# Optimization experiments

Measured on AMD Instinct MI355X. Metric: run time of the kernel, lower is better.

The kernel has to match this reference:

```python
import jax, jax.numpy as jnp
from jax import lax
import numpy as np

B, D, L = 32, 64, 4096
E = 8          # num_experts
K = 2          # top-k
OC = 32        # out_channels


def setup_inputs() -> dict:
    key = jax.random.key(0)
    ks = jax.random.split(key, 6)
    x = jax.random.normal(ks[0], (B, D, L), dtype=jnp.float32)
    # gating weight [D*5, E] (torch init is zeros; use small random for a meaningful reference)
    w_gate = jax.random.normal(ks[1], (D * 5, E), dtype=jnp.float32) * 0.02
    # Conv1d(D -> OC, kernel 3)
    conv1_w = jax.random.normal(ks[2], (OC, D, 3), dtype=jnp.float32) * (1.0 / np.sqrt(D * 3))
    conv1_b = jax.random.normal(ks[3], (OC,), dtype=jnp.float32) * 0.01
    # Conv1d(OC -> OC*E, kernel 1)
    conv2_w = jax.random.normal(ks[4], (OC * E, OC, 1), dtype=jnp.float32) * (1.0 / np.sqrt(OC))
    conv2_b = jax.random.normal(ks[5], (OC * E,), dtype=jnp.float32) * 0.01
    return {"x": x, "w_gate": w_gate, "conv1_w": conv1_w, "conv1_b": conv1_b,
            "conv2_w": conv2_w, "conv2_b": conv2_b}


def _gates(g_in, w_gate):
    # eval-mode noisy_top_k_gating: no noise, softmax -> top-(k+1) -> renormalize top-k -> scatter
    logits = jax.nn.softmax(g_in @ w_gate, axis=1)            # [B, E]
    top_v, top_i = lax.top_k(logits, min(K + 1, E))           # sorted descending
    vk = top_v[:, :K]
    ik = top_i[:, :K]
    gk = vk / (jnp.sum(vk, axis=1, keepdims=True) + 1e-6)
    gates = jnp.zeros_like(logits).at[jnp.arange(logits.shape[0])[:, None], ik].set(gk)
    return gates


def reference(x, w_gate, conv1_w, conv1_b, conv2_w, conv2_b):
    b, d, l = x.shape
    g_in = x[:, :, -6:-1].reshape(b, d * 5)                   # last-5-timestep gating features
    gates = _gates(g_in, w_gate)                              # [B, E]
    dn = ("NCH", "OIH", "NCH")
    h = lax.conv_general_dilated(x, conv1_w, (1,), "VALID", dimension_numbers=dn)
    h = jnp.tanh(h + conv1_b[None, :, None])                  # [B, OC, L-2]
    out = lax.conv_general_dilated(h, conv2_w, (1,), "VALID", dimension_numbers=dn)
    out = out + conv2_b[None, :, None]                        # [B, OC*E, L']
    lp = out.shape[-1]
    out = out.transpose(0, 2, 1).reshape(b, lp, OC, E)        # [B, L', OC, E]
    moe = jnp.einsum("blde,be->bld", out, gates)              # weighted combine
    return moe.transpose(0, 2, 1)                             # [B, OC, L']
```

## Files before the change

kernel.cpp:

```cpp
#include <hip/hip_runtime.h>
#include <math.h>

#define B_  32
#define D_  64
#define L_  4096
#define E_  8
#define OC_ 32
#define LP_ 4094
#define TILE 128
#define NT   32

typedef __attribute__((ext_vector_type(8)))  short short8;
typedef __attribute__((ext_vector_type(16))) float float16;

static __device__ __forceinline__ unsigned cvtpk(float a, float b) {
    unsigned r;
    asm("v_cvt_pk_bf16_f32 %0, %1, %2" : "=v"(r) : "v"(a), "v"(b));
    return r;
}
static __device__ __forceinline__ float fast_tanh(float x) {
    float e = __expf(2.0f * x);
    return fmaf(-2.0f, __builtin_amdgcn_rcpf(e + 1.0f), 1.0f);
}

__global__ __launch_bounds__(256, 4)
void fused_all(const float* __restrict__ x,
               const float* __restrict__ w_gate,
               const float* __restrict__ c1w,
               const float* __restrict__ c1b,
               const float* __restrict__ c2w,
               const float* __restrict__ c2b,
               float* __restrict__ out)
{
    __shared__ __align__(16) unsigned short xT[130 * 64];
    __shared__ __align__(16) unsigned short aFl[12 * 64 * 8];

    const int tid  = threadIdx.x;
    const int lane = tid & 63;
    const int wv   = tid >> 6;
    const int b    = blockIdx.x >> 5;
    const int l0   = (blockIdx.x & 31) << 7;
    const float* xb = x + (size_t)b * (D_ * L_);

    {
        const int c2 = tid >> 3;
        const int jb = (tid & 7) << 2;
        const float* p0 = xb + (size_t)(2 * c2) * L_ + l0;
        const float* p1 = p0 + L_;
        #pragma unroll
        for (int jq = 0; jq < 4; ++jq) {
            int j = jq * 32 + jb;
            float4 v0 = *(const float4*)(p0 + j);
            float4 v1 = *(const float4*)(p1 + j);
            float e0[4] = {v0.x, v0.y, v0.z, v0.w};
            float e1[4] = {v1.x, v1.y, v1.z, v1.w};
            #pragma unroll
            for (int r = 0; r < 4; ++r) {
                int row = j + r;
                int off = (row * 128 + c2 * 4) ^ ((row & 7) << 4);
                *(unsigned*)((char*)xT + off) = cvtpk(e0[r], e1[r]);
            }
        }
        if (tid < 64) {
            int cc2 = tid >> 1, jj = tid & 1;
            int row = TILE + jj;
            int lg  = l0 + row;
            float f0 = 0.f, f1 = 0.f;
            if (lg < L_) {
                f0 = xb[(size_t)(2 * cc2) * L_ + lg];
                f1 = xb[(size_t)(2 * cc2 + 1) * L_ + lg];
            }
            int off = (row * 128 + cc2 * 4) ^ ((row & 7) << 4);
            *(unsigned*)((char*)xT + off) = cvtpk(f0, f1);
        }
    }

    {
        const int oc = tid >> 3;
        const int c0 = (tid & 7) << 3;
        const float* wp = c1w + oc * 192 + c0 * 3;
        float v[24];
        #pragma unroll
        for (int q = 0; q < 6; ++q)
            *(float4*)(v + 4 * q) = *(const float4*)(wp + 4 * q);
        const int ksoff = c0 >> 4;
        const int half  = (c0 >> 3) & 1;
        #pragma unroll
        for (int t = 0; t < 3; ++t) {
            union { short8 s8; unsigned u[4]; } w8;
            #pragma unroll
            for (int jj = 0; jj < 4; ++jj)
                w8.u[jj] = cvtpk(v[(2 * jj) * 3 + t], v[(2 * jj + 1) * 3 + t]);
            int base = ((t * 4 + ksoff) * 64 + half * 32 + oc) * 8;
            *(short8*)(aFl + base) = w8.s8;
        }
    }

    int i0, i1;
    float g0, g1;
    {
        const int d = lane;
        float part[E_];
        #pragma unroll
        for (int e = 0; e < E_; ++e) part[e] = 0.f;
        #pragma unroll
        for (int t = 0; t < 5; ++t) {
            float xvt = xb[(size_t)d * L_ + (L_ - 6) + t];
            const float* wgp = w_gate + (d * 5 + t) * E_;
            float4 wa = *(const float4*)wgp;
            float4 wb = *(const float4*)(wgp + 4);
            part[0] = fmaf(xvt, wa.x, part[0]);
            part[1] = fmaf(xvt, wa.y, part[1]);
            part[2] = fmaf(xvt, wa.z, part[2]);
            part[3] = fmaf(xvt, wa.w, part[3]);
            part[4] = fmaf(xvt, wb.x, part[4]);
            part[5] = fmaf(xvt, wb.y, part[5]);
            part[6] = fmaf(xvt, wb.z, part[6]);
            part[7] = fmaf(xvt, wb.w, part[7]);
        }
        #pragma unroll
        for (int off = 1; off < 64; off <<= 1) {
            #pragma unroll
            for (int e = 0; e < E_; ++e)
                part[e] += __shfl_xor(part[e], off, 64);
        }
        float m = part[0];
        #pragma unroll
        for (int e = 1; e < E_; ++e) m = fmaxf(m, part[e]);
        float p[E_], s = 0.f;
        #pragma unroll
        for (int e = 0; e < E_; ++e) { p[e] = expf(part[e] - m); s += p[e]; }
        float inv = 1.f / s;
        #pragma unroll
        for (int e = 0; e < E_; ++e) p[e] *= inv;

        i0 = 0;
        #pragma unroll
        for (int e = 1; e < E_; ++e) if (p[e] > p[i0]) i0 = e;
        i1 = (i0 == 0) ? 1 : 0;
        #pragma unroll
        for (int e = 0; e < E_; ++e) {
            if (e == i0) continue;
            if (p[e] > p[i1]) i1 = e;
        }
        const float v0 = p[i0], v1 = p[i1];
        const float den = v0 + v1 + 1e-6f;
        g0 = v0 / den;
        g1 = v1 / den;
    }

    const int cl = lane & 31;
    const int hi = lane >> 5;

    short8 a2[2];
    #pragma unroll
    for (int ks = 0; ks < 2; ++ks) {
        const float* q0 = c2w + (cl * E_ + i0) * OC_ + ks * 16 + hi * 8;
        const float* q1 = c2w + (cl * E_ + i1) * OC_ + ks * 16 + hi * 8;
        float4 u0a = *(const float4*)q0, u0b = *(const float4*)(q0 + 4);
        float4 u1a = *(const float4*)q1, u1b = *(const float4*)(q1 + 4);
        union { short8 s8; unsigned u[4]; } f;
        f.u[0] = cvtpk(fmaf(g0, u0a.x, g1 * u1a.x), fmaf(g0, u0a.y, g1 * u1a.y));
        f.u[1] = cvtpk(fmaf(g0, u0a.z, g1 * u1a.z), fmaf(g0, u0a.w, g1 * u1a.w));
        f.u[2] = cvtpk(fmaf(g0, u0b.x, g1 * u1b.x), fmaf(g0, u0b.y, g1 * u1b.y));
        f.u[3] = cvtpk(fmaf(g0, u0b.z, g1 * u1b.z), fmaf(g0, u0b.w, g1 * u1b.w));
        a2[ks] = f.s8;
    }

    __syncthreads();

    const int cb = wv * 32;
    float16 acc = (float16)0.0f;
    #pragma unroll
    for (int t = 0; t < 3; ++t) {
        int row = cb + cl + t;
        int rb  = row * 128;
        int swz = (row & 7) << 4;
        #pragma unroll
        for (int q = 0; q < 4; ++q) {
            short8 af = *(const short8*)(aFl + ((t * 4 + q) * 64 + lane) * 8);
            int off = (rb + q * 32 + hi * 16) ^ swz;
            short8 bf = *(const short8*)((const char*)xT + off);
            acc = __builtin_amdgcn_mfma_f32_32x32x16_bf16(af, bf, acc, 0, 0, 0);
        }
    }

    float th[16];
    #pragma unroll
    for (int r = 0; r < 16; ++r) {
        int row = (r & 3) + 8 * (r >> 2) + 4 * hi;
        th[r] = fast_tanh(acc[r] + c1b[row]);
    }

    unsigned x0a = hi ? cvtpk(th[0],  th[1])  : cvtpk(th[4],  th[5]);
    unsigned x0b = hi ? cvtpk(th[2],  th[3])  : cvtpk(th[6],  th[7]);
    unsigned x1a = hi ? cvtpk(th[8],  th[9])  : cvtpk(th[12], th[13]);
    unsigned x1b = hi ? cvtpk(th[10], th[11]) : cvtpk(th[14], th[15]);
    unsigned r0a = (unsigned)__shfl_xor((int)x0a, 32, 64);
    unsigned r0b = (unsigned)__shfl_xor((int)x0b, 32, 64);
    unsigned r1a = (unsigned)__shfl_xor((int)x1a, 32, 64);
    unsigned r1b = (unsigned)__shfl_xor((int)x1b, 32, 64);

    union U { short8 s8; unsigned u[4]; };
    U b0, b1;
    b0.u[0] = hi ? r0a : cvtpk(th[0], th[1]);
    b0.u[1] = hi ? r0b : cvtpk(th[2], th[3]);
    b0.u[2] = hi ? cvtpk(th[4], th[5]) : r0a;
    b0.u[3] = hi ? cvtpk(th[6], th[7]) : r0b;
    b1.u[0] = hi ? r1a : cvtpk(th[8], th[9]);
    b1.u[1] = hi ? r1b : cvtpk(th[10], th[11]);
    b1.u[2] = hi ? cvtpk(th[12], th[13]) : r1a;
    b1.u[3] = hi ? cvtpk(th[14], th[15]) : r1b;

    float16 acc2 = (float16)0.0f;
    acc2 = __builtin_amdgcn_mfma_f32_32x32x16_bf16(a2[0], b0.s8, acc2, 0, 0, 0);
    acc2 = __builtin_amdgcn_mfma_f32_32x32x16_bf16(a2[1], b1.s8, acc2, 0, 0, 0);

    int l = l0 + cb + cl;
    if (l < LP_) {
        float* ob = out + (size_t)b * (OC_ * (size_t)LP_) + l;
        #pragma unroll
        for (int r = 0; r < 16; ++r) {
            int row = (r & 3) + 8 * (r >> 2) + 4 * hi;
            float bb = fmaf(g0, c2b[row * E_ + i0], g1 * c2b[row * E_ + i1]);
            ob[(size_t)row * LP_] = acc2[r] + bb;
        }
    }
}

extern "C" void kernel_launch(void* const* d_in, const int* in_sizes, int n_in,
                              void* d_out, int out_size, void* d_ws, size_t ws_size,
                              hipStream_t stream)
{
    const float* x      = (const float*)d_in[0];
    const float* w_gate = (const float*)d_in[1];
    const float* c1w    = (const float*)d_in[2];
    const float* c1b    = (const float*)d_in[3];
    const float* c2w    = (const float*)d_in[4];
    const float* c2b    = (const float*)d_in[5];
    float* out = (float*)d_out;

    fused_all<<<B_ * NT, 256, 0, stream>>>(x, w_gate, c1w, c1b, c2w, c2b, out);
}
```

Baseline: 22.75 us.

## Issue all global loads up front and compute gating on one wave via LDS

All global loads of the x tile, the halo and the conv1 weights are issued into registers at kernel start, before the gating computation, so their latency overlaps the gating math. The gating softmax/top-k and the mixing of the conv2 weights now run only on wave 0, with the results shared to the other waves through LDS instead of being computed redundantly by every wave. The conv1 A-fragments are preloaded from LDS into registers before the MFMA loop. This raises register pressure, which could lower occupancy, and adds LDS traffic for broadcasting the gate values.

```diff
diff --git a/kernel.cpp b/kernel.cpp
--- a/kernel.cpp
+++ b/kernel.cpp
@@ -7,8 +7,6 @@
 #define E_  8
 #define OC_ 32
 #define LP_ 4094
-#define TILE 128
-#define NT   32
 
 typedef __attribute__((ext_vector_type(8)))  short short8;
 typedef __attribute__((ext_vector_type(16))) float float16;
@@ -32,8 +30,11 @@
                const float* __restrict__ c2b,
                float* __restrict__ out)
 {
-    __shared__ __align__(16) unsigned short xT[130 * 64];
+    __shared__ __align__(16) unsigned short xT[132 * 64];
     __shared__ __align__(16) unsigned short aFl[12 * 64 * 8];
+    __shared__ __align__(16) unsigned short a2L[2 * 64 * 8];
+    __shared__ float gF[2];
+    __shared__ int   gI[2];
 
     const int tid  = threadIdx.x;
     const int lane = tid & 63;
@@ -42,63 +43,38 @@
     const int l0   = (blockIdx.x & 31) << 7;
     const float* xb = x + (size_t)b * (D_ * L_);
 
+    const int c2 = tid >> 3;
+    const int jb = (tid & 7) << 2;
+    const float* p0 = xb + (size_t)(2 * c2) * L_ + l0;
+    const float* p1 = p0 + L_;
+    float4 A0[4], A1[4];
+    #pragma unroll
+    for (int jq = 0; jq < 4; ++jq) {
+        int j = jq * 32 + jb;
+        A0[jq] = *(const float4*)(p0 + j);
+        A1[jq] = *(const float4*)(p1 + j);
+    }
+    float hA0 = 0.f, hA1 = 0.f;
+    const int haloc = tid >> 1, haloj = tid & 1;
+    if (tid < 64) {
+        int lg = l0 + 128 + haloj;
+        if (lg < L_) {
+            hA0 = xb[(size_t)(2 * haloc) * L_ + lg];
+            hA1 = xb[(size_t)(2 * haloc + 1) * L_ + lg];
+        }
+    }
+
+    const int w_oc = tid >> 3;
+    const int w_c0 = (tid & 7) << 3;
+    float wv24[24];
     {
-        const int c2 = tid >> 3;
-        const int jb = (tid & 7) << 2;
-        const float* p0 = xb + (size_t)(2 * c2) * L_ + l0;
-        const float* p1 = p0 + L_;
-        #pragma unroll
-        for (int jq = 0; jq < 4; ++jq) {
-            int j = jq * 32 + jb;
-            float4 v0 = *(const float4*)(p0 + j);
-            float4 v1 = *(const float4*)(p1 + j);
-            float e0[4] = {v0.x, v0.y, v0.z, v0.w};
-            float e1[4] = {v1.x, v1.y, v1.z, v1.w};
-            #pragma unroll
-            for (int r = 0; r < 4; ++r) {
-                int row = j + r;
-                int off = (row * 128 + c2 * 4) ^ ((row & 7) << 4);
-                *(unsigned*)((char*)xT + off) = cvtpk(e0[r], e1[r]);
-            }
-        }
-        if (tid < 64) {
-            int cc2 = tid >> 1, jj = tid & 1;
-            int row = TILE + jj;
-            int lg  = l0 + row;
-            float f0 = 0.f, f1 = 0.f;
-            if (lg < L_) {
-                f0 = xb[(size_t)(2 * cc2) * L_ + lg];
-                f1 = xb[(size_t)(2 * cc2 + 1) * L_ + lg];
-            }
-            int off = (row * 128 + cc2 * 4) ^ ((row & 7) << 4);
-            *(unsigned*)((char*)xT + off) = cvtpk(f0, f1);
-        }
-    }
-
-    {
-        const int oc = tid >> 3;
-        const int c0 = (tid & 7) << 3;
-        const float* wp = c1w + oc * 192 + c0 * 3;
-        float v[24];
+        const float* wp = c1w + w_oc * 192 + w_c0 * 3;
         #pragma unroll
         for (int q = 0; q < 6; ++q)
-            *(float4*)(v + 4 * q) = *(const float4*)(wp + 4 * q);
-        const int ksoff = c0 >> 4;
-        const int half  = (c0 >> 3) & 1;
-        #pragma unroll
-        for (int t = 0; t < 3; ++t) {
-            union { short8 s8; unsigned u[4]; } w8;
-            #pragma unroll
-            for (int jj = 0; jj < 4; ++jj)
-                w8.u[jj] = cvtpk(v[(2 * jj) * 3 + t], v[(2 * jj + 1) * 3 + t]);
-            int base = ((t * 4 + ksoff) * 64 + half * 32 + oc) * 8;
-            *(short8*)(aFl + base) = w8.s8;
-        }
-    }
-
-    int i0, i1;
-    float g0, g1;
-    {
+            *(float4*)(wv24 + 4 * q) = *(const float4*)(wp + 4 * q);
+    }
+
+    if (wv == 0) {
         const int d = lane;
         float part[E_];
         #pragma unroll
@@ -134,10 +110,10 @@
         #pragma unroll
         for (int e = 0; e < E_; ++e) p[e] *= inv;
 
-        i0 = 0;
+        int i0 = 0;
         #pragma unroll
         for (int e = 1; e < E_; ++e) if (p[e] > p[i0]) i0 = e;
-        i1 = (i0 == 0) ? 1 : 0;
+        int i1 = (i0 == 0) ? 1 : 0;
         #pragma unroll
         for (int e = 0; e < E_; ++e) {
             if (e == i0) continue;
@@ -145,29 +121,73 @@
         }
         const float v0 = p[i0], v1 = p[i1];
         const float den = v0 + v1 + 1e-6f;
-        g0 = v0 / den;
-        g1 = v1 / den;
-    }
+        const float g0 = v0 / den, g1 = v1 / den;
+
+        const int cl0 = lane & 31;
+        const int hi0 = lane >> 5;
+        #pragma unroll
+        for (int ks = 0; ks < 2; ++ks) {
+            const float* q0 = c2w + (cl0 * E_ + i0) * OC_ + ks * 16 + hi0 * 8;
+            const float* q1 = c2w + (cl0 * E_ + i1) * OC_ + ks * 16 + hi0 * 8;
+            float4 u0a = *(const float4*)q0, u0b = *(const float4*)(q0 + 4);
+            float4 u1a = *(const float4*)q1, u1b = *(const float4*)(q1 + 4);
+            union { short8 s8; unsigned u[4]; } f;
+            f.u[0] = cvtpk(fmaf(g0, u0a.x, g1 * u1a.x), fmaf(g0, u0a.y, g1 * u1a.y));
+            f.u[1] = cvtpk(fmaf(g0, u0a.z, g1 * u1a.z), fmaf(g0, u0a.w, g1 * u1a.w));
+            f.u[2] = cvtpk(fmaf(g0, u0b.x, g1 * u1b.x), fmaf(g0, u0b.y, g1 * u1b.y));
+            f.u[3] = cvtpk(fmaf(g0, u0b.z, g1 * u1b.z), fmaf(g0, u0b.w, g1 * u1b.w));
+            *(short8*)(a2L + (ks * 64 + lane) * 8) = f.s8;
+        }
+        if (lane == 0) {
+            gF[0] = g0; gF[1] = g1;
+            gI[0] = i0; gI[1] = i1;
+        }
+    }
+
+    {
+        const int ksoff = w_c0 >> 4;
+        const int half  = (w_c0 >> 3) & 1;
+        #pragma unroll
+        for (int t = 0; t < 3; ++t) {
+            union { short8 s8; unsigned u[4]; } w8;
+            #pragma unroll
+            for (int jj = 0; jj < 4; ++jj)
+                w8.u[jj] = cvtpk(wv24[(2 * jj) * 3 + t], wv24[(2 * jj + 1) * 3 + t]);
+            int base = ((t * 4 + ksoff) * 64 + half * 32 + w_oc) * 8;
+            *(short8*)(aFl + base) = w8.s8;
+        }
+    }
+
+    #pragma unroll
+    for (int jq = 0; jq < 4; ++jq) {
+        float e0[4] = {A0[jq].x, A0[jq].y, A0[jq].z, A0[jq].w};
+        float e1[4] = {A1[jq].x, A1[jq].y, A1[jq].z, A1[jq].w};
+        #pragma unroll
+        for (int r = 0; r < 4; ++r) {
+            int row = jq * 32 + jb + r;
+            int off = (row * 128 + c2 * 4) ^ ((row & 7) << 4);
+            *(unsigned*)((char*)xT + off) = cvtpk(e0[r], e1[r]);
+        }
+    }
+    if (tid < 64) {
+        int row = 128 + haloj;
+        int off = (row * 128 + haloc * 4) ^ ((row & 7) << 4);
+        *(unsigned*)((char*)xT + off) = cvtpk(hA0, hA1);
+    }
+
+    __syncthreads();
 
     const int cl = lane & 31;
     const int hi = lane >> 5;
-
+    short8 a1[12];
+    #pragma unroll
+    for (int ks = 0; ks < 12; ++ks)
+        a1[ks] = *(const short8*)(aFl + (ks * 64 + lane) * 8);
     short8 a2[2];
-    #pragma unroll
-    for (int ks = 0; ks < 2; ++ks) {
-        const float* q0 = c2w + (cl * E_ + i0) * OC_ + ks * 16 + hi * 8;
-        const float* q1 = c2w + (cl * E_ + i1) * OC_ + ks * 16 + hi * 8;
-        float4 u0a = *(const float4*)q0, u0b = *(const float4*)(q0 + 4);
-        float4 u1a = *(const float4*)q1, u1b = *(const float4*)(q1 + 4);
-        union { short8 s8; unsigned u[4]; } f;
-        f.u[0] = cvtpk(fmaf(g0, u0a.x, g1 * u1a.x), fmaf(g0, u0a.y, g1 * u1a.y));
-        f.u[1] = cvtpk(fmaf(g0, u0a.z, g1 * u1a.z), fmaf(g0, u0a.w, g1 * u1a.w));
-        f.u[2] = cvtpk(fmaf(g0, u0b.x, g1 * u1b.x), fmaf(g0, u0b.y, g1 * u1b.y));
-        f.u[3] = cvtpk(fmaf(g0, u0b.z, g1 * u1b.z), fmaf(g0, u0b.w, g1 * u1b.w));
-        a2[ks] = f.s8;
-    }
-
-    __syncthreads();
+    a2[0] = *(const short8*)(a2L + (0 * 64 + lane) * 8);
+    a2[1] = *(const short8*)(a2L + (1 * 64 + lane) * 8);
+    const float g0 = gF[0], g1 = gF[1];
+    const int   i0 = gI[0], i1 = gI[1];
 
     const int cb = wv * 32;
     float16 acc = (float16)0.0f;
@@ -178,10 +198,9 @@
         int swz = (row & 7) << 4;
         #pragma unroll
         for (int q = 0; q < 4; ++q) {
-            short8 af = *(const short8*)(aFl + ((t * 4 + q) * 64 + lane) * 8);
             int off = (rb + q * 32 + hi * 16) ^ swz;
             short8 bf = *(const short8*)((const char*)xT + off);
-            acc = __builtin_amdgcn_mfma_f32_32x32x16_bf16(af, bf, acc, 0, 0, 0);
+            acc = __builtin_amdgcn_mfma_f32_32x32x16_bf16(a1[t * 4 + q], bf, acc, 0, 0, 0);
         }
     }
 
@@ -240,5 +259,5 @@
     const float* c2b    = (const float*)d_in[5];
     float* out = (float*)d_out;
 
-    fused_all<<<B_ * NT, 256, 0, stream>>>(x, w_gate, c1w, c1b, c2w, c2b, out);
-}
+    fused_all<<<B_ * 32, 256, 0, stream>>>(x, w_gate, c1w, c1b, c2w, c2b, out);
+}
```

Measured after the change: 20.05 us. 1.13x faster.
